# Kernel tuning notes

Measured on AMD Instinct MI355X. Metric: run time of the kernel, lower is better.

## Reference

```python
import jax, jax.numpy as jnp
import numpy as np

N_OP, N_TAB, N_COL, N_PRED = 131072, 32768, 131072, 65536
NCF = 32
H = 512
NUM_GRAPHS = 64
EPS = 1e-5  # torch LayerNorm default
# fixed relation order: (src_type, dst_type)
RELS = [('table', 'operator'), ('predicate', 'operator'), ('column', 'operator'),
        ('column', 'predicate'), ('operator', 'operator'), ('table', 'table'), ('column', 'column')]
NNODE = {'operator': N_OP, 'table': N_TAB, 'column': N_COL, 'predicate': N_PRED}
EDGES = [262144, 262144, 262144, 262144, 262144, 32768, 131072]


def setup_inputs() -> dict:
    key = jax.random.key(0)
    ks = iter(jax.random.split(key, 80))
    def nrm(shape, fan_in):
        return jax.random.normal(next(ks), shape, jnp.float32) / np.sqrt(fan_in).astype(np.float32)
    inp = {
        'x_operator': jax.random.normal(next(ks), (N_OP, 4), jnp.float32),
        'x_table': jax.random.normal(next(ks), (N_TAB, 2), jnp.float32),
        'x_column': jax.random.normal(next(ks), (N_COL, NCF), jnp.float32),
        'x_predicate': jax.random.normal(next(ks), (N_PRED, 4), jnp.float32),
        'W_op': nrm((4, H), 4), 'b_op': jnp.zeros((H,), jnp.float32),
        'W_tab': nrm((2, H), 2), 'b_tab': jnp.zeros((H,), jnp.float32),
        'W_col': nrm((NCF, H), NCF), 'b_col': jnp.zeros((H,), jnp.float32),
        'W_pred': nrm((4, H), 4), 'b_pred': jnp.zeros((H,), jnp.float32),
        'conv1_Wl': nrm((7, H, H), H), 'conv1_bl': jnp.zeros((7, H), jnp.float32),
        'conv1_Wr': nrm((7, H, H), H),
        'conv2_Wl': nrm((7, H, H), H), 'conv2_bl': jnp.zeros((7, H), jnp.float32),
        'conv2_Wr': nrm((7, H, H), H),
        'g1': jnp.ones((H,), jnp.float32), 'beta1': jnp.zeros((H,), jnp.float32),
        'g2': jnp.ones((H,), jnp.float32), 'beta2': jnp.zeros((H,), jnp.float32),
        'W_out': nrm((H, 1), H), 'b_out': jnp.zeros((1,), jnp.float32),
    }
    for i, (s, d) in enumerate(RELS):
        e = EDGES[i]
        inp[f'src{i}'] = jax.random.randint(next(ks), (e,), 0, NNODE[s], jnp.int32)
        inp[f'dst{i}'] = jax.random.randint(next(ks), (e,), 0, NNODE[d], jnp.int32)
    inp['batch_operator'] = jnp.sort(jax.random.randint(next(ks), (N_OP,), 0, NUM_GRAPHS, jnp.int32))
    return inp


def _layer_norm(x, g, b):
    m = jnp.mean(x, -1, keepdims=True)
    v = jnp.mean((x - m) ** 2, -1, keepdims=True)
    return (x - m) * jax.lax.rsqrt(v + EPS) * g + b


def _segment_mean(vals, idx, n):
    s = jax.ops.segment_sum(vals, idx, num_segments=n)
    c = jax.ops.segment_sum(jnp.ones(idx.shape, vals.dtype), idx, num_segments=n)
    return s / jnp.maximum(c, 1.0)[:, None]


def _sage(x_src, x_dst, src, dst, Wl, bl, Wr, n_dst):
    # PyG SAGEConv: lin_l(mean of neighbor msgs) + lin_r(root), lin_r has no bias
    agg = _segment_mean(x_src[src], dst, n_dst)
    return agg @ Wl + bl + x_dst @ Wr


def _forward(x_operator, x_table, x_column, x_predicate,
             W_op, b_op, W_tab, b_tab, W_col, b_col, W_pred, b_pred,
             conv1_Wl, conv1_bl, conv1_Wr, conv2_Wl, conv2_bl, conv2_Wr,
             g1, beta1, g2, beta2, W_out, b_out, edges, batch_operator):
    h = {'operator': x_operator @ W_op + b_op,
         'table': x_table @ W_tab + b_tab,
         'column': x_column @ W_col + b_col,
         'predicate': x_predicate @ W_pred + b_pred}

    def hetero(h, Wl, bl, Wr):
        outs = {}
        for i, (s, d) in enumerate(RELS):
            src, dst = edges[i]
            o = _sage(h[s], h[d], src, dst, Wl[i], bl[i], Wr[i], NNODE[d])
            outs.setdefault(d, []).append(o)
        # HeteroConv aggr='mean' across relations sharing a dst node type
        return {k: sum(v) / len(v) for k, v in outs.items()}

    h = hetero(h, conv1_Wl, conv1_bl, conv1_Wr)
    h = {k: _layer_norm(jax.nn.elu(v), g1, beta1) for k, v in h.items()}  # dropout = eval identity
    h = hetero(h, conv2_Wl, conv2_bl, conv2_Wr)
    h = {k: _layer_norm(jax.nn.elu(v), g2, beta2) for k, v in h.items()}
    pooled = _segment_mean(h['operator'], batch_operator, NUM_GRAPHS)  # global_mean_pool
    return (pooled @ W_out + b_out).squeeze()


def reference(x_operator, x_table, x_column, x_predicate,
              W_op, b_op, W_tab, b_tab, W_col, b_col, W_pred, b_pred,
              conv1_Wl, conv1_bl, conv1_Wr, conv2_Wl, conv2_bl, conv2_Wr,
              g1, beta1, g2, beta2, W_out, b_out,
              src0, dst0, src1, dst1, src2, dst2, src3, dst3,
              src4, dst4, src5, dst5, src6, dst6, batch_operator):
    edges = [(src0, dst0), (src1, dst1), (src2, dst2), (src3, dst3),
             (src4, dst4), (src5, dst5), (src6, dst6)]
    return _forward(x_operator, x_table, x_column, x_predicate,
                    W_op, b_op, W_tab, b_tab, W_col, b_col, W_pred, b_pred,
                    conv1_Wl, conv1_bl, conv1_Wr, conv2_Wl, conv2_bl, conv2_Wr,
                    g1, beta1, g2, beta2, W_out, b_out, edges, batch_operator)
```

## Files before the change

### kernel.cpp

```cpp
#include <hip/hip_runtime.h>
#include <hip/hip_bf16.h>

typedef unsigned short u16;
typedef __attribute__((ext_vector_type(8))) short bf16x8;
typedef __attribute__((ext_vector_type(4))) short bf16x4;
typedef __attribute__((ext_vector_type(4))) float f32x4;

typedef __attribute__((address_space(1))) const void gv_t;
typedef __attribute__((address_space(3))) void lv_t;

#define DEVINL __device__ __forceinline__

DEVINL float bf2f(u16 s) { union { unsigned u; float f; } v; v.u = ((unsigned)s) << 16; return v.f; }
DEVINL u16 f2bf(float f) {
  union { float f; unsigned u; } v; v.f = f;
  return (u16)((v.u + 0x7FFFu + ((v.u >> 16) & 1u)) >> 16);
}

__global__ void probe_k(float* __restrict__ out, float v) { out[threadIdx.x] = v; }

struct PackPtrs { const float* wl2; const float* wr2; const float* g1; u16* bt[5]; };
__global__ __launch_bounds__(256) void pack_multi(PackPtrs p) {
  int j = blockIdx.x >> 10;
  int idx = (blockIdx.x & 1023) * 256 + threadIdx.x;
  int k = idx >> 9, n = idx & 511;
  float v;
  if (j < 4) {
    int r = (j == 3) ? 4 : j;
    v = p.wl2[((size_t)r * 512 + k) * 512 + n];
  } else {
    size_t o = (size_t)k * 512 + n;
    v = p.wr2[o] + p.wr2[o + 262144] + p.wr2[o + 524288] + p.wr2[o + 1048576];
  }
  p.bt[j][(size_t)n * 512 + k] = f2bf(v * 0.25f * p.g1[k]);
}

__global__ __launch_bounds__(256) void csbb_k(const float* __restrict__ wl2,
                                              const float* __restrict__ wr2,
                                              const float* __restrict__ g1,
                                              const float* __restrict__ be1,
                                              float* __restrict__ cs, float* __restrict__ bb) {
  __shared__ float redA[256], redB[256];
  int j = blockIdx.x >> 4;
  int n = (blockIdx.x & 15) * 32 + (threadIdx.x & 31);
  int kg = threadIdx.x >> 5;
  float a = 0.f, b = 0.f;
  for (int k = kg * 64; k < kg * 64 + 64; ++k) {
    float w;
    if (j < 4) {
      int r = (j == 3) ? 4 : j;
      w = wl2[((size_t)r * 512 + k) * 512 + n];
    } else {
      size_t o = (size_t)k * 512 + n;
      w = wr2[o] + wr2[o + 262144] + wr2[o + 524288] + wr2[o + 1048576];
    }
    a += g1[k] * w;
    b += be1[k] * w;
  }
  redA[threadIdx.x] = a;
  redB[threadIdx.x] = b;
  __syncthreads();
  if (kg == 0) {
    float va = 0.f, vb = 0.f;
#pragma unroll
    for (int q = 0; q < 8; ++q) {
      va += redA[(threadIdx.x & 31) + q * 32];
      vb += redB[(threadIdx.x & 31) + q * 32];
    }
    cs[j * 512 + n] = va * 0.25f;
    bb[j * 512 + n] = vb * 0.25f;
  }
}

struct FoldPtrs { const float* a[8]; const float* w[2]; u16* bt[4]; };
__constant__ int   c_off[19] = {0,16,24,56,64,320,328,360,368,400,416,424,440,696,704,960,1216,1224,1256};
__constant__ int   c_ai[18]  = {0,1,2,3,4,5,6,7,6, 0,1,0, 4,5,4, 4,5,2};
__constant__ int   c_wi[18]  = {0,0,0,0,0,0,0,0,1, 0,0,1, 0,0,1, 0,0,1};
__constant__ int   c_r0[18]  = {0,0,1,1,2,2,4,4,0, 5,5,5, 6,6,6, 3,3,3};
__constant__ float c_sc[18]  = {0.25f,0.25f,0.25f,0.25f,0.25f,0.25f,0.25f,0.25f,0.25f,
                                1.f,1.f,1.f, 1.f,1.f,1.f, 1.f,1.f,1.f};
__constant__ int   c_bt[18]  = {0,0,0,0,0,0,0,0,0, 1,1,1, 2,2,2, 3,3,3};
__constant__ int   c_K[18]   = {64,64,64,64,64,64,64,64,64, 64,64,64, 128,128,128, 64,64,64};
__constant__ int   c_ko[18]  = {0,2,3,7,8,40,41,45,46, 0,2,3, 0,32,33, 0,32,33};

__global__ __launch_bounds__(256) void fold_multi(FoldPtrs p) {
  __shared__ float red[256];
  int b = blockIdx.x;
  int j = 0;
#pragma unroll
  for (int t = 1; t < 18; ++t) j += (b >= c_off[t]);
  int rel = b - c_off[j];
  int f = rel >> 3, nb = rel & 7;
  int tid = threadIdx.x;
  int n = nb * 64 + (tid & 63);
  int kg = tid >> 6;
  const float* A = p.a[c_ai[j]] + (size_t)f * 512;
  const float* W = p.w[c_wi[j]];
  int k0 = kg * 128;
  float acc = 0.f;
  if (j != 8) {
    const float* Wp = W + (size_t)c_r0[j] * 512 * 512 + n;
#pragma unroll 16
    for (int k = k0; k < k0 + 128; ++k) acc += A[k] * Wp[(size_t)k * 512];
  } else {
    const float* W0 = W + n;
    const float* W1 = W + (size_t)262144 + n;
    const float* W2 = W + (size_t)524288 + n;
    const float* W4 = W + (size_t)1048576 + n;
#pragma unroll 8
    for (int k = k0; k < k0 + 128; ++k) {
      size_t o = (size_t)k * 512;
      acc += A[k] * (W0[o] + W1[o] + W2[o] + W4[o]);
    }
  }
  red[tid] = acc;
  __syncthreads();
  if (kg == 0) {
    float v = red[tid] + red[tid + 64] + red[tid + 128] + red[tid + 192];
    p.bt[c_bt[j]][(size_t)n * c_K[j] + c_ko[j] + f] = f2bf(v * c_sc[j]);
  }
}

struct VFPtrs { const float* bl[5]; const float* bvec[5]; const float* w; float* out[5]; };
__constant__ int   c_vi[5][4] = {{0,1,2,4},{0,1,2,4},{5,-1,-1,-1},{6,-1,-1,-1},{3,-1,-1,-1}};
__constant__ float c_vs[5]    = {0.25f,0.25f,1.f,1.f,1.f};

__global__ __launch_bounds__(256) void vecfold_multi(VFPtrs p) {
  __shared__ float red[256];
  int j = blockIdx.x >> 4, blk = blockIdx.x & 15;
  int tid = threadIdx.x;
  int n = blk * 32 + (tid & 31);
  int kg = tid >> 5;
  const float* bv = p.bvec[j];
  float a = 0.f;
  if (bv) {
    int i1 = c_vi[j][1];
    const float* W0 = p.w + (size_t)c_vi[j][0] * 262144 + n;
    if (i1 < 0) {
#pragma unroll 16
      for (int k = kg * 64; k < kg * 64 + 64; ++k) a += bv[k] * W0[(size_t)k * 512];
    } else {
      const float* W1 = p.w + (size_t)c_vi[j][1] * 262144 + n;
      const float* W2 = p.w + (size_t)c_vi[j][2] * 262144 + n;
      const float* W3 = p.w + (size_t)c_vi[j][3] * 262144 + n;
#pragma unroll 8
      for (int k = kg * 64; k < kg * 64 + 64; ++k) {
        size_t o = (size_t)k * 512;
        a += bv[k] * (W0[o] + W1[o] + W2[o] + W3[o]);
      }
    }
  }
  red[tid] = a;
  __syncthreads();
  if (kg == 0) {
    float v = 0.f;
#pragma unroll
    for (int q = 0; q < 8; ++q) v += red[(tid & 31) + q * 32];
    float bsum = p.bl[j][c_vi[j][0] * 512 + n];
    if (c_vi[j][1] >= 0) {
      bsum += p.bl[j][c_vi[j][1] * 512 + n];
      bsum += p.bl[j][c_vi[j][2] * 512 + n];
      bsum += p.bl[j][c_vi[j][3] * 512 + n];
    }
    p.out[j][n] = (v + bsum) * c_vs[j];
  }
}

struct EdgePtrs { const int* dst[7]; const int* src[7]; };
__constant__ int c_hoff[8]  = {0,1024,2048,3072,4096,5120,5248,5760};
__constant__ int c_hbase[7] = {0,131072,262144,393216,458752,589824,622592};
__constant__ int c_hne[7]   = {262144,262144,262144,262144,262144,32768,131072};

__global__ __launch_bounds__(256) void hist_multi(EdgePtrs p, int* __restrict__ cnt) {
  int b = blockIdx.x;
  int j = 0;
#pragma unroll
  for (int t = 1; t < 7; ++t) j += (b >= c_hoff[t]);
  int i = (b - c_hoff[j]) * 256 + threadIdx.x;
  if (i < c_hne[j]) atomicAdd(&cnt[c_hbase[j] + p.dst[j][i]], 1);
}

__global__ __launch_bounds__(256) void fill_multi(EdgePtrs p, int* __restrict__ cursor,
                                                  int* __restrict__ esrc) {
  int b = blockIdx.x;
  int j = 0;
#pragma unroll
  for (int t = 1; t < 7; ++t) j += (b >= c_hoff[t]);
  int i = (b - c_hoff[j]) * 256 + threadIdx.x;
  if (i < c_hne[j]) {
    int pos = atomicAdd(&cursor[c_hbase[j] + p.dst[j][i]], 1);
    esrc[pos] = p.src[j][i];
  }
}

__global__ void scan1_k(const int* __restrict__ in, int* __restrict__ out,
                        int* __restrict__ part, int n) {
  __shared__ int s[256];
  int t = threadIdx.x;
  int base = blockIdx.x * 1024 + t * 4;
  int x0 = 0, x1 = 0, x2 = 0, x3 = 0;
  if (base < n) x0 = in[base];
  if (base + 1 < n) x1 = in[base + 1];
  if (base + 2 < n) x2 = in[base + 2];
  if (base + 3 < n) x3 = in[base + 3];
  int tsum = x0 + x1 + x2 + x3;
  s[t] = tsum;
  __syncthreads();
  for (int off = 1; off < 256; off <<= 1) {
    int v = (t >= off) ? s[t - off] : 0;
    __syncthreads();
    s[t] += v;
    __syncthreads();
  }
  int excl = s[t] - tsum;
  if (base < n) out[base] = excl;
  if (base + 1 < n) out[base + 1] = excl + x0;
  if (base + 2 < n) out[base + 2] = excl + x0 + x1;
  if (base + 3 < n) out[base + 3] = excl + x0 + x1 + x2;
  if (t == 255) part[blockIdx.x] = s[255];
}

__global__ void scan2_k(int* __restrict__ part, int nb) {
  __shared__ int s[1024];
  int t = threadIdx.x;
  int orig = (t < nb) ? part[t] : 0;
  s[t] = orig;
  __syncthreads();
  for (int off = 1; off < 1024; off <<= 1) {
    int v = (t >= off) ? s[t - off] : 0;
    __syncthreads();
    s[t] += v;
    __syncthreads();
  }
  if (t < nb) part[t] = s[t] - orig;
}

__global__ void scan3_k(int* __restrict__ out, int* __restrict__ cursor,
                        const int* __restrict__ part, int n) {
  int i = blockIdx.x * 256 + threadIdx.x;
  if (i < n) {
    int v = out[i] + part[i >> 10];
    out[i] = v;
    cursor[i] = v;
  }
}

__global__ void raw_agg(const int* __restrict__ offs, const int* __restrict__ esrc,
                        const float* __restrict__ x, int F, u16* __restrict__ A1,
                        int K, int colOff, int indCol, int nd) {
  int row = blockIdx.x * 32 + (threadIdx.x >> 3);
  if (row >= nd) return;
  int j = threadIdx.x & 7;
  int e0 = offs[row], e1 = offs[row + 1];
  float acc[4] = {0.f, 0.f, 0.f, 0.f};
  for (int e = e0; e < e1; ++e) {
    int s = esrc[e];
#pragma unroll
    for (int u = 0; u < 4; ++u) {
      int f = j + u * 8;
      if (f < F) acc[u] += x[(size_t)s * F + f];
    }
  }
  float inv = (e1 > e0) ? 1.f / (float)(e1 - e0) : 0.f;
#pragma unroll
  for (int u = 0; u < 4; ++u) {
    int f = j + u * 8;
    if (f < F) A1[(size_t)row * K + colOff + f] = f2bf(acc[u] * inv);
  }
  if (j == 0) A1[(size_t)row * K + indCol] = f2bf((e1 > e0) ? 1.f : 0.f);
}

struct RawPtrs { const int* offs; const int* esrc; const float* x[4]; u16* A1; };
__constant__ int c_gF[4]    = {2,4,32,4};
__constant__ int c_gco[4]   = {0,3,8,41};
__constant__ int c_gic[4]   = {2,7,40,45};
__constant__ int c_gcsrb[4] = {0,131072,262144,458752};

__global__ __launch_bounds__(256) void raw_multi(RawPtrs p, int s0) {
  int j = blockIdx.x >> 10;
  int row = (blockIdx.x & 1023) * 32 + (threadIdx.x >> 3);
  int jj = threadIdx.x & 7;
  const int* offs = p.offs + c_gcsrb[j] + s0;
  const float* x = p.x[j];
  int F = c_gF[j];
  int e0 = offs[row], e1 = offs[row + 1];
  float acc[4] = {0.f, 0.f, 0.f, 0.f};
  for (int e = e0; e < e1; ++e) {
    int s = p.esrc[e];
#pragma unroll
    for (int u = 0; u < 4; ++u) {
      int f = jj + u * 8;
      if (f < F) acc[u] += x[(size_t)s * F + f];
    }
  }
  float inv = (e1 > e0) ? 1.f / (float)(e1 - e0) : 0.f;
#pragma unroll
  for (int u = 0; u < 4; ++u) {
    int f = jj + u * 8;
    if (f < F) p.A1[(size_t)row * 64 + c_gco[j] + f] = f2bf(acc[u] * inv);
  }
  if (jj == 0) p.A1[(size_t)row * 64 + c_gic[j]] = f2bf((e1 > e0) ? 1.f : 0.f);
}

__global__ void a1_root(const float* __restrict__ x, int rowBase, u16* __restrict__ A1,
                        int K, int rootOff, int nd, int lf) {
  int idx = blockIdx.x * 256 + threadIdx.x;
  int i = idx >> lf, f = idx & ((1 << lf) - 1);
  if (i >= nd) return;
  A1[(size_t)i * K + rootOff + f] = f2bf(x[(((size_t)(rowBase + i)) << lf) + f]);
}

template <bool FIRST>
__global__ __launch_bounds__(256) void gather_acc(
    const int* __restrict__ offs, const int* __restrict__ esrc,
    const u16* __restrict__ hT, const float* __restrict__ bias,
    u16* __restrict__ acc, int s0, int s1) {
  int w = blockIdx.x * 4 + (threadIdx.x >> 6);
  int l = threadIdx.x & 63;
  int e0 = offs[w], e1 = offs[w + 1];
  float sum[8] = {0.f, 0.f, 0.f, 0.f, 0.f, 0.f, 0.f, 0.f};
  bool found = false;
  for (int e = e0; e < e1; ++e) {
    int s = esrc[e];
    if (s >= s0 && s < s1) {
      found = true;
      bf16x8 v = *(const bf16x8*)&hT[(size_t)(s - s0) * 512 + l * 8];
#pragma unroll
      for (int j = 0; j < 8; ++j) sum[j] += bf2f((u16)v[j]);
    }
  }
  float inv = (e1 > e0) ? 1.f / (float)(e1 - e0) : 0.f;
  u16* ap = acc + (size_t)w * 512 + l * 8;
  bf16x8 r;
  if (FIRST) {
#pragma unroll
    for (int j = 0; j < 8; ++j) r[j] = (short)f2bf(bias[l * 8 + j] + sum[j] * inv);
    *(bf16x8*)ap = r;
  } else {
    if (!found) return;
    bf16x8 old = *(const bf16x8*)ap;
#pragma unroll
    for (int j = 0; j < 8; ++j) r[j] = (short)f2bf(bf2f((u16)old[j]) + sum[j] * inv);
    *(bf16x8*)ap = r;
  }
}

template <bool ELU, int K>
__global__ __launch_bounds__(256) void gemm_k(
    const u16* __restrict__ A, const u16* __restrict__ BT,
    const float* __restrict__ bias, u16* __restrict__ C) {
  __shared__ u16 As[128 * 64];
  __shared__ u16 Bs[128 * 64];
  int b = blockIdx.x;
  int u = (b & 7) * 128 + (b >> 3);
  int bm = (u >> 2) * 128;
  int bn = (u & 3) * 128;
  int tid = threadIdx.x;
  int wid = tid >> 6, lane = tid & 63;
  int wm = wid >> 1, wn = wid & 1;
  int r16 = lane & 15, hi4 = lane >> 4;
  int srow = tid >> 3;
  int scol = ((tid & 7) ^ (srow & 7)) * 8;
  int sw = r16 & 7;
  f32x4 acc[4][4];
#pragma unroll
  for (int i = 0; i < 4; ++i)
#pragma unroll
    for (int j = 0; j < 4; ++j) acc[i][j] = (f32x4){0.f, 0.f, 0.f, 0.f};

#pragma unroll
  for (int k0 = 0; k0 < K; k0 += 64) {
    __syncthreads();
#pragma unroll
    for (int i = 0; i < 4; ++i) {
      const u16* ga = A + (size_t)(bm + i * 32 + srow) * K + k0 + scol;
      const u16* gb = BT + (size_t)(bn + i * 32 + srow) * K + k0 + scol;
      __builtin_amdgcn_global_load_lds((gv_t*)ga, (lv_t*)(As + i * 2048 + wid * 512), 16, 0, 0);
      __builtin_amdgcn_global_load_lds((gv_t*)gb, (lv_t*)(Bs + i * 2048 + wid * 512), 16, 0, 0);
    }
    __syncthreads();
#pragma unroll
    for (int kk = 0; kk < 64; kk += 32) {
      bf16x8 af[4], bfr[4];
#pragma unroll
      for (int f = 0; f < 4; ++f) {
        int grp = (kk >> 3) + hi4;
        af[f]  = *(const bf16x8*)&As[(wm * 64 + f * 16 + r16) * 64 + ((grp ^ sw) << 3)];
        bfr[f] = *(const bf16x8*)&Bs[(wn * 64 + f * 16 + r16) * 64 + ((grp ^ sw) << 3)];
      }
#pragma unroll
      for (int mf = 0; mf < 4; ++mf)
#pragma unroll
        for (int nf = 0; nf < 4; ++nf)
          acc[mf][nf] = __builtin_amdgcn_mfma_f32_16x16x32_bf16(bfr[nf], af[mf], acc[mf][nf], 0, 0, 0);
    }
  }
#pragma unroll
  for (int mf = 0; mf < 4; ++mf) {
    int r = bm + wm * 64 + mf * 16 + r16;
#pragma unroll
    for (int nf = 0; nf < 4; ++nf) {
      int c0 = bn + wn * 64 + nf * 16 + hi4 * 4;
      u16* cp = C + (size_t)r * 512 + c0;
      f32x4 bv = *(const f32x4*)&bias[c0];
      bf16x4 res;
#pragma unroll
      for (int j = 0; j < 4; ++j) {
        float v = acc[mf][nf][j] + bv[j];
        if (ELU) v = v > 0.f ? v : expm1f(v);
        res[j] = (short)f2bf(v);
      }
      *(bf16x4*)cp = res;
    }
  }
}

__global__ void ln_stats(const u16* __restrict__ H, float2* __restrict__ stats, int rows) {
  int w = blockIdx.x * 4 + (threadIdx.x >> 6);
  if (w >= rows) return;
  int l = threadIdx.x & 63;
  bf16x8 v = *(const bf16x8*)&H[(size_t)w * 512 + l * 8];
  float x[8];
  float s = 0.f;
#pragma unroll
  for (int j = 0; j < 8; ++j) { x[j] = bf2f((u16)v[j]); s += x[j]; }
#pragma unroll
  for (int m = 1; m < 64; m <<= 1) s += __shfl_xor(s, m, 64);
  float mean = s * (1.f / 512.f);
  float q = 0.f;
#pragma unroll
  for (int j = 0; j < 8; ++j) { float d = x[j] - mean; q += d * d; }
#pragma unroll
  for (int m = 1; m < 64; m <<= 1) q += __shfl_xor(q, m, 64);
  if (l == 0) stats[w] = make_float2(mean, rsqrtf(q * (1.f / 512.f) + 1e-5f));
}

template <bool ACC>
__global__ __launch_bounds__(256) void gemm_t(
    const u16* __restrict__ A, const u16* __restrict__ BT, u16* __restrict__ C,
    const float2* __restrict__ stats, const float* __restrict__ cs,
    const float* __restrict__ bb) {
  __shared__ u16 As[128 * 64];
  __shared__ u16 Bs[128 * 64];
  int b = blockIdx.x;
  int u = (b & 7) * 128 + (b >> 3);
  int bm = (u >> 2) * 128;
  int bn = (u & 3) * 128;
  int tid = threadIdx.x;
  int wid = tid >> 6, lane = tid & 63;
  int wm = wid >> 1, wn = wid & 1;
  int r16 = lane & 15, hi4 = lane >> 4;
  int srow = tid >> 3;
  int scol = ((tid & 7) ^ (srow & 7)) * 8;
  int sw = r16 & 7;
  f32x4 acc[4][4];
#pragma unroll
  for (int i = 0; i < 4; ++i)
#pragma unroll
    for (int j = 0; j < 4; ++j) acc[i][j] = (f32x4){0.f, 0.f, 0.f, 0.f};

#pragma unroll
  for (int k0 = 0; k0 < 512; k0 += 64) {
    __syncthreads();
#pragma unroll
    for (int i = 0; i < 4; ++i) {
      const u16* ga = A + (size_t)(bm + i * 32 + srow) * 512 + k0 + scol;
      const u16* gb = BT + (size_t)(bn + i * 32 + srow) * 512 + k0 + scol;
      __builtin_amdgcn_global_load_lds((gv_t*)ga, (lv_t*)(As + i * 2048 + wid * 512), 16, 0, 0);
      __builtin_amdgcn_global_load_lds((gv_t*)gb, (lv_t*)(Bs + i * 2048 + wid * 512), 16, 0, 0);
    }
    __syncthreads();
#pragma unroll
    for (int kk = 0; kk < 64; kk += 32) {
      bf16x8 af[4], bfr[4];
#pragma unroll
      for (int f = 0; f < 4; ++f) {
        int grp = (kk >> 3) + hi4;
        af[f]  = *(const bf16x8*)&As[(wm * 64 + f * 16 + r16) * 64 + ((grp ^ sw) << 3)];
        bfr[f] = *(const bf16x8*)&Bs[(wn * 64 + f * 16 + r16) * 64 + ((grp ^ sw) << 3)];
      }
#pragma unroll
      for (int mf = 0; mf < 4; ++mf)
#pragma unroll
        for (int nf = 0; nf < 4; ++nf)
          acc[mf][nf] = __builtin_amdgcn_mfma_f32_16x16x32_bf16(bfr[nf], af[mf], acc[mf][nf], 0, 0, 0);
    }
  }
#pragma unroll
  for (int mf = 0; mf < 4; ++mf) {
    int r = bm + wm * 64 + mf * 16 + r16;
    float2 st = stats[r];
    float mr = st.x * st.y;
#pragma unroll
    for (int nf = 0; nf < 4; ++nf) {
      int c0 = bn + wn * 64 + nf * 16 + hi4 * 4;
      u16* cp = C + (size_t)r * 512 + c0;
      f32x4 csv = *(const f32x4*)&cs[c0];
      f32x4 bbv = *(const f32x4*)&bb[c0];
      bf16x4 res;
      if (ACC) {
        bf16x4 oldv = *(const bf16x4*)cp;
#pragma unroll
        for (int j = 0; j < 4; ++j) {
          float v = st.y * acc[mf][nf][j] - mr * csv[j] + bbv[j] + bf2f((u16)oldv[j]);
          res[j] = (short)f2bf(v);
        }
      } else {
#pragma unroll
        for (int j = 0; j < 4; ++j) {
          float v = st.y * acc[mf][nf][j] - mr * csv[j] + bbv[j];
          res[j] = (short)f2bf(v);
        }
      }
      *(bf16x4*)cp = res;
    }
  }
}

DEVINL int lowb(const int* a, int n, int v) {
  int lo = 0, hi = n;
  while (lo < hi) { int m = (lo + hi) >> 1; if (a[m] < v) lo = m + 1; else hi = m; }
  return lo;
}

__global__ __launch_bounds__(256) void pool1v(const u16* __restrict__ H,
                                              const int* __restrict__ batch, int nOp,
                                              const float* __restrict__ g2,
                                              const float* __restrict__ be2,
                                              float* __restrict__ pooled,
                                              int* __restrict__ cnts) {
  __shared__ float red[4][512];
  int gr = blockIdx.x >> 4, part = blockIdx.x & 15;
  int lo = lowb(batch, nOp, gr), hi = lowb(batch, nOp, gr + 1);
  if (part == 0 && threadIdx.x == 0) cnts[gr] = hi - lo;
  int len = hi - lo;
  int chunk = (len + 15) >> 4;
  int r0 = lo + part * chunk;
  int r1 = r0 + chunk;
  if (r1 > hi) r1 = hi;
  int wv = threadIdx.x >> 6, l = threadIdx.x & 63;
  float a[8] = {0.f, 0.f, 0.f, 0.f, 0.f, 0.f, 0.f, 0.f};
  float gv[8], bv[8];
#pragma unroll
  for (int j = 0; j < 8; ++j) { gv[j] = g2[l * 8 + j]; bv[j] = be2[l * 8 + j]; }
  for (int r = r0 + wv; r < r1; r += 4) {
    bf16x8 v = *(const bf16x8*)&H[(size_t)r * 512 + l * 8];
    float x[8];
    float s = 0.f;
#pragma unroll
    for (int j = 0; j < 8; ++j) {
      x[j] = bf2f((u16)v[j]);
      x[j] = x[j] > 0.f ? x[j] : expm1f(x[j]);
      s += x[j];
    }
#pragma unroll
    for (int m = 1; m < 64; m <<= 1) s += __shfl_xor(s, m, 64);
    float mean = s * (1.f / 512.f);
    float q = 0.f;
#pragma unroll
    for (int j = 0; j < 8; ++j) { float d = x[j] - mean; q += d * d; }
#pragma unroll
    for (int m = 1; m < 64; m <<= 1) q += __shfl_xor(q, m, 64);
    float rsd = rsqrtf(q * (1.f / 512.f) + 1e-5f);
#pragma unroll
    for (int j = 0; j < 8; ++j) a[j] += (x[j] - mean) * rsd * gv[j] + bv[j];
  }
#pragma unroll
  for (int j = 0; j < 8; ++j) red[wv][l * 8 + j] = a[j];
  __syncthreads();
  if (wv == 0) {
#pragma unroll
    for (int j = 0; j < 8; ++j) {
      int c = l * 8 + j;
      float s = red[0][c] + red[1][c] + red[2][c] + red[3][c];
      atomicAdd(&pooled[gr * 512 + c], s);
    }
  }
}

__global__ void pool2(const float* __restrict__ pooled, const int* __restrict__ cnts,
                      const float* __restrict__ Wout, const float* __restrict__ bout,
                      float* __restrict__ out) {
  int gg = blockIdx.x;
  int l = threadIdx.x;
  float s = 0.f;
#pragma unroll
  for (int j = 0; j < 8; ++j) {
    int c = l * 8 + j;
    s += pooled[gg * 512 + c] * Wout[c];
  }
#pragma unroll
  for (int m = 1; m < 64; m <<= 1) s += __shfl_xor(s, m, 64);
  if (l == 0) {
    int c = cnts[gg];
    if (c < 1) c = 1;
    out[gg] = s / (float)c + bout[0];
  }
}

extern "C" void kernel_launch(void* const* d_in, const int* in_sizes, int n_in,
                              void* d_out, int out_size, void* d_ws, size_t ws_size,
                              hipStream_t stream) {
  (void)in_sizes; (void)n_in; (void)out_size;
  const float* x_op   = (const float*)d_in[0];
  const float* x_tab  = (const float*)d_in[1];
  const float* x_col  = (const float*)d_in[2];
  const float* x_pred = (const float*)d_in[3];
  const float* W_op = (const float*)d_in[4],  *b_op = (const float*)d_in[5];
  const float* W_tab = (const float*)d_in[6], *b_tab = (const float*)d_in[7];
  const float* W_col = (const float*)d_in[8], *b_col = (const float*)d_in[9];
  const float* W_pred = (const float*)d_in[10], *b_pred = (const float*)d_in[11];
  const float* Wl1 = (const float*)d_in[12];
  const float* bl1 = (const float*)d_in[13];
  const float* Wr1 = (const float*)d_in[14];
  const float* Wl2 = (const float*)d_in[15];
  const float* bl2 = (const float*)d_in[16];
  const float* Wr2 = (const float*)d_in[17];
  const float* g1  = (const float*)d_in[18];
  const float* be1 = (const float*)d_in[19];
  const float* g2  = (const float*)d_in[20];
  const float* be2 = (const float*)d_in[21];
  const float* Wout = (const float*)d_in[22];
  const float* bout = (const float*)d_in[23];
  const int* SRC[7], *DST[7];
  for (int r = 0; r < 7; ++r) { SRC[r] = (const int*)d_in[24 + 2 * r]; DST[r] = (const int*)d_in[25 + 2 * r]; }
  const int* batch = (const int*)d_in[38];
  float* out = (float*)d_out;

  const int CSRB[7] = {0, 131072, 262144, 393216, 458752, 589824, 622592};
  const int TOT = 753664;
  const int NOP = 131072;

  char* ws = (char*)d_ws;
  u16* acc     = (u16*)ws;
  u16* h1      = (u16*)(ws + 134217728ull);
  int* curFul  = (int*)(ws + 134217728ull);
  u16* hT      = (u16*)(ws + 167772160ull);
  u16* A1      = (u16*)(ws + 234881024ull);
  int* offsFul = (int*)(ws + 243269632ull);
  int* esrcFul = (int*)(ws + 246284544ull);
  u16* BT2_0   = (u16*)(ws + 252182784ull);
  u16* BT2_1   = BT2_0 + 262144;
  u16* BT2_2   = BT2_1 + 262144;
  u16* BT2_4   = BT2_2 + 262144;
  u16* BT2rt   = BT2_4 + 262144;
  u16* BT1op   = (u16*)(ws + 254804224ull);
  u16* BT1tab  = (u16*)(ws + 254869760ull);
  u16* BT1col  = (u16*)(ws + 254935296ull);
  u16* BT1pr   = (u16*)(ws + 255066368ull);
  float* b1op  = (float*)(ws + 255131904ull);
  float* b1tab = b1op + 512, *b1col = b1op + 1024, *b1pr = b1op + 1536, *b2vec = b1op + 2048;
  float* pooled = (float*)(ws + 255142144ull);
  int* cnts     = (int*)(ws + 255273216ull);
  int* part     = (int*)(ws + 255273472ull);
  float2* stats = (float2*)(ws + 255277568ull);
  float* cs     = (float*)(ws + 255539712ull);
  float* bb     = (float*)(ws + 255549952ull);
  const size_t WS_NEED = 255560192ull;
  if (ws_size < WS_NEED) { probe_k<<<1, 64, 0, stream>>>(out, (float)ws_size); return; }

  (void)hipMemsetAsync(curFul, 0, 3014912ull, stream);
  EdgePtrs ep;
  for (int r = 0; r < 7; ++r) { ep.dst[r] = DST[r]; ep.src[r] = SRC[r]; }
  hist_multi<<<5760, 256, 0, stream>>>(ep, curFul);
  scan1_k<<<737, 256, 0, stream>>>(curFul, offsFul, part, TOT + 1);
  scan2_k<<<1, 1024, 0, stream>>>(part, 737);
  scan3_k<<<2945, 256, 0, stream>>>(offsFul, curFul, part, TOT + 1);
  fill_multi<<<5760, 256, 0, stream>>>(ep, curFul, esrcFul);

  PackPtrs pp;
  pp.wl2 = Wl2; pp.wr2 = Wr2; pp.g1 = g1;
  pp.bt[0] = BT2_0; pp.bt[1] = BT2_1; pp.bt[2] = BT2_2; pp.bt[3] = BT2_4; pp.bt[4] = BT2rt;
  pack_multi<<<5120, 256, 0, stream>>>(pp);
  csbb_k<<<80, 256, 0, stream>>>(Wl2, Wr2, g1, be1, cs, bb);
  (void)hipMemsetAsync(BT1op, 0, 65536 + 65536 + 131072 + 65536, stream);
  FoldPtrs fp;
  fp.a[0] = W_tab; fp.a[1] = b_tab; fp.a[2] = W_pred; fp.a[3] = b_pred;
  fp.a[4] = W_col; fp.a[5] = b_col; fp.a[6] = W_op;   fp.a[7] = b_op;
  fp.w[0] = Wl1;   fp.w[1] = Wr1;
  fp.bt[0] = BT1op; fp.bt[1] = BT1tab; fp.bt[2] = BT1col; fp.bt[3] = BT1pr;
  fold_multi<<<1256, 256, 0, stream>>>(fp);
  VFPtrs vp;
  vp.bl[0] = bl2; vp.bl[1] = bl1; vp.bl[2] = bl1; vp.bl[3] = bl1; vp.bl[4] = bl1;
  vp.bvec[0] = nullptr; vp.bvec[1] = b_op; vp.bvec[2] = b_tab; vp.bvec[3] = b_col; vp.bvec[4] = b_pred;
  vp.w = Wr1;
  vp.out[0] = b2vec; vp.out[1] = b1op; vp.out[2] = b1tab; vp.out[3] = b1col; vp.out[4] = b1pr;
  vecfold_multi<<<80, 256, 0, stream>>>(vp);

  float* cs0 = cs, *cs1 = cs + 512, *cs2 = cs + 1024, *cs4 = cs + 1536, *csrt = cs + 2048;
  float* bb0 = bb, *bb1 = bb + 512, *bb2 = bb + 1024, *bb4 = bb + 1536, *bbrt = bb + 2048;

  (void)hipMemsetAsync(A1, 0, 32768ull * 64 * 2, stream);
  raw_agg<<<1024, 256, 0, stream>>>(offsFul + CSRB[5], esrcFul, x_tab, 2, A1, 64, 0, 2, 32768);
  a1_root<<<256, 256, 0, stream>>>(x_tab, 0, A1, 64, 3, 32768, 1);
  gemm_k<true, 64><<<1024, 256, 0, stream>>>(A1, BT1tab, b1tab, h1);
  ln_stats<<<8192, 256, 0, stream>>>(h1, stats, 32768);
  gemm_t<false><<<1024, 256, 0, stream>>>(h1, BT2_0, hT, stats, cs0, bb0);
  gather_acc<true><<<32768, 256, 0, stream>>>(offsFul + CSRB[0], esrcFul, hT, b2vec, acc, 0, 32768);

  (void)hipMemsetAsync(A1, 0, 32768ull * 64 * 2, stream);
  for (int q = 0; q < 2; ++q) {
    int qs = q * 32768;
    raw_agg<<<1024, 256, 0, stream>>>(offsFul + CSRB[3] + qs, esrcFul, x_col, 32, A1, 64, 0, 32, 32768);
    a1_root<<<512, 256, 0, stream>>>(x_pred, qs, A1, 64, 33, 32768, 2);
    gemm_k<true, 64><<<1024, 256, 0, stream>>>(A1, BT1pr, b1pr, h1);
    ln_stats<<<8192, 256, 0, stream>>>(h1, stats, 32768);
    gemm_t<false><<<1024, 256, 0, stream>>>(h1, BT2_1, hT + (size_t)qs * 512, stats, cs1, bb1);
  }
  gather_acc<false><<<32768, 256, 0, stream>>>(offsFul + CSRB[1], esrcFul, hT, nullptr, acc, 0, 65536);

  (void)hipMemsetAsync(A1, 0, 32768ull * 128 * 2, stream);
  for (int hs = 0; hs < 2; ++hs) {
    int S0 = hs * 65536;
    for (int q = 0; q < 2; ++q) {
      int qs = S0 + q * 32768;
      raw_agg<<<1024, 256, 0, stream>>>(offsFul + CSRB[6] + qs, esrcFul, x_col, 32, A1, 128, 0, 32, 32768);
      a1_root<<<4096, 256, 0, stream>>>(x_col, qs, A1, 128, 33, 32768, 5);
      gemm_k<true, 128><<<1024, 256, 0, stream>>>(A1, BT1col, b1col, h1);
      ln_stats<<<8192, 256, 0, stream>>>(h1, stats, 32768);
      gemm_t<false><<<1024, 256, 0, stream>>>(h1, BT2_2, hT + (size_t)q * 32768 * 512, stats, cs2, bb2);
    }
    gather_acc<false><<<32768, 256, 0, stream>>>(offsFul + CSRB[2], esrcFul, hT, nullptr,
                                                 acc, S0, S0 + 65536);
  }

  (void)hipMemsetAsync(A1, 0, 32768ull * 64 * 2, stream);
  for (int hs = 0; hs < 2; ++hs) {
    int S0 = hs * 65536;
    for (int q = 0; q < 2; ++q) {
      int qs = S0 + q * 32768;
      RawPtrs rp;
      rp.offs = offsFul; rp.esrc = esrcFul; rp.A1 = A1;
      rp.x[0] = x_tab; rp.x[1] = x_pred; rp.x[2] = x_col; rp.x[3] = x_op;
      raw_multi<<<4096, 256, 0, stream>>>(rp, qs);
      a1_root<<<512, 256, 0, stream>>>(x_op, qs, A1, 64, 46, 32768, 2);
      gemm_k<true, 64><<<1024, 256, 0, stream>>>(A1, BT1op, b1op, h1);
      ln_stats<<<8192, 256, 0, stream>>>(h1, stats, 32768);
      gemm_t<true><<<1024, 256, 0, stream>>>(h1, BT2rt, acc + (size_t)qs * 512, stats, csrt, bbrt);
      gemm_t<false><<<1024, 256, 0, stream>>>(h1, BT2_4, hT + (size_t)q * 32768 * 512, stats, cs4, bb4);
    }
    gather_acc<false><<<32768, 256, 0, stream>>>(offsFul + CSRB[4], esrcFul, hT, nullptr,
                                                 acc, S0, S0 + 65536);
  }

  (void)hipMemsetAsync(pooled, 0, 64 * 512 * 4, stream);
  pool1v<<<1024, 256, 0, stream>>>(acc, batch, NOP, g2, be2, pooled, cnts);
  pool2<<<64, 64, 0, stream>>>(pooled, cnts, Wout, bout, out);
}
```

Baseline: 1.614 ms.

## Partition CSR build atomics by destination range and merge operator gemm_t launches

The histogram and fill kernels now launch eight times as many blocks, and each block handles only edges whose destination index falls in one of eight ranges. The aim is to keep each block's atomics on a narrower, more cache-local region of the counter array, at the cost of every edge index being read eight times. Separately, the two gemm_t launches for the operator root and operator-operator relation are fused into one 2048-block kernel, which removes a launch and lets both GEMMs run concurrently on the same h1 input.

Result: faster. 1.561 ms (-3.3%).

```diff
diff --git a/kernel.cpp b/kernel.cpp
--- a/kernel.cpp
+++ b/kernel.cpp
@@ -171,25 +171,37 @@
 __constant__ int c_hbase[7] = {0,131072,262144,393216,458752,589824,622592};
 __constant__ int c_hne[7]   = {262144,262144,262144,262144,262144,32768,131072};
 
-__global__ __launch_bounds__(256) void hist_multi(EdgePtrs p, int* __restrict__ cnt) {
-  int b = blockIdx.x;
-  int j = 0;
-#pragma unroll
-  for (int t = 1; t < 7; ++t) j += (b >= c_hoff[t]);
-  int i = (b - c_hoff[j]) * 256 + threadIdx.x;
-  if (i < c_hne[j]) atomicAdd(&cnt[c_hbase[j] + p.dst[j][i]], 1);
-}
-
-__global__ __launch_bounds__(256) void fill_multi(EdgePtrs p, int* __restrict__ cursor,
-                                                  int* __restrict__ esrc) {
-  int b = blockIdx.x;
-  int j = 0;
-#pragma unroll
-  for (int t = 1; t < 7; ++t) j += (b >= c_hoff[t]);
-  int i = (b - c_hoff[j]) * 256 + threadIdx.x;
-  if (i < c_hne[j]) {
-    int pos = atomicAdd(&cursor[c_hbase[j] + p.dst[j][i]], 1);
-    esrc[pos] = p.src[j][i];
+__global__ __launch_bounds__(256) void hist8(EdgePtrs p, int* __restrict__ cnt) {
+  int range = blockIdx.x & 7;
+  int lo = range * 94208, hi = lo + 94208;
+  for (int chunk = blockIdx.x >> 3; chunk < 5760; chunk += 4096) {
+    int j = 0;
+#pragma unroll
+    for (int t = 1; t < 7; ++t) j += (chunk >= c_hoff[t]);
+    int i = (chunk - c_hoff[j]) * 256 + threadIdx.x;
+    if (i < c_hne[j]) {
+      int idx = c_hbase[j] + p.dst[j][i];
+      if (idx >= lo && idx < hi) atomicAdd(&cnt[idx], 1);
+    }
+  }
+}
+
+__global__ __launch_bounds__(256) void fill8(EdgePtrs p, int* __restrict__ cursor,
+                                             int* __restrict__ esrc) {
+  int range = blockIdx.x & 7;
+  int lo = range * 94208, hi = lo + 94208;
+  for (int chunk = blockIdx.x >> 3; chunk < 5760; chunk += 4096) {
+    int j = 0;
+#pragma unroll
+    for (int t = 1; t < 7; ++t) j += (chunk >= c_hoff[t]);
+    int i = (chunk - c_hoff[j]) * 256 + threadIdx.x;
+    if (i < c_hne[j]) {
+      int idx = c_hbase[j] + p.dst[j][i];
+      if (idx >= lo && idx < hi) {
+        int pos = atomicAdd(&cursor[idx], 1);
+        esrc[pos] = p.src[j][i];
+      }
+    }
   }
 }
 
@@ -499,6 +511,93 @@
       f32x4 bbv = *(const f32x4*)&bb[c0];
       bf16x4 res;
       if (ACC) {
+        bf16x4 oldv = *(const bf16x4*)cp;
+#pragma unroll
+        for (int j = 0; j < 4; ++j) {
+          float v = st.y * acc[mf][nf][j] - mr * csv[j] + bbv[j] + bf2f((u16)oldv[j]);
+          res[j] = (short)f2bf(v);
+        }
+      } else {
+#pragma unroll
+        for (int j = 0; j < 4; ++j) {
+          float v = st.y * acc[mf][nf][j] - mr * csv[j] + bbv[j];
+          res[j] = (short)f2bf(v);
+        }
+      }
+      *(bf16x4*)cp = res;
+    }
+  }
+}
+
+__global__ __launch_bounds__(256) void gemm_t2(
+    const u16* __restrict__ A, const u16* __restrict__ BTrt, const u16* __restrict__ BT4,
+    u16* __restrict__ Cacc, u16* __restrict__ ChT, const float2* __restrict__ stats,
+    const float* __restrict__ csrt, const float* __restrict__ bbrt,
+    const float* __restrict__ cs4, const float* __restrict__ bb4) {
+  __shared__ u16 As[128 * 64];
+  __shared__ u16 Bs[128 * 64];
+  bool second = blockIdx.x >= 1024;
+  const u16* BT = second ? BT4 : BTrt;
+  u16* C = second ? ChT : Cacc;
+  const float* cs = second ? cs4 : csrt;
+  const float* bb = second ? bb4 : bbrt;
+  int b = blockIdx.x & 1023;
+  int u = (b & 7) * 128 + (b >> 3);
+  int bm = (u >> 2) * 128;
+  int bn = (u & 3) * 128;
+  int tid = threadIdx.x;
+  int wid = tid >> 6, lane = tid & 63;
+  int wm = wid >> 1, wn = wid & 1;
+  int r16 = lane & 15, hi4 = lane >> 4;
+  int srow = tid >> 3;
+  int scol = ((tid & 7) ^ (srow & 7)) * 8;
+  int sw = r16 & 7;
+  f32x4 acc[4][4];
+#pragma unroll
+  for (int i = 0; i < 4; ++i)
+#pragma unroll
+    for (int j = 0; j < 4; ++j) acc[i][j] = (f32x4){0.f, 0.f, 0.f, 0.f};
+
+#pragma unroll
+  for (int k0 = 0; k0 < 512; k0 += 64) {
+    __syncthreads();
+#pragma unroll
+    for (int i = 0; i < 4; ++i) {
+      const u16* ga = A + (size_t)(bm + i * 32 + srow) * 512 + k0 + scol;
+      const u16* gb = BT + (size_t)(bn + i * 32 + srow) * 512 + k0 + scol;
+      __builtin_amdgcn_global_load_lds((gv_t*)ga, (lv_t*)(As + i * 2048 + wid * 512), 16, 0, 0);
+      __builtin_amdgcn_global_load_lds((gv_t*)gb, (lv_t*)(Bs + i * 2048 + wid * 512), 16, 0, 0);
+    }
+    __syncthreads();
+#pragma unroll
+    for (int kk = 0; kk < 64; kk += 32) {
+      bf16x8 af[4], bfr[4];
+#pragma unroll
+      for (int f = 0; f < 4; ++f) {
+        int grp = (kk >> 3) + hi4;
+        af[f]  = *(const bf16x8*)&As[(wm * 64 + f * 16 + r16) * 64 + ((grp ^ sw) << 3)];
+        bfr[f] = *(const bf16x8*)&Bs[(wn * 64 + f * 16 + r16) * 64 + ((grp ^ sw) << 3)];
+      }
+#pragma unroll
+      for (int mf = 0; mf < 4; ++mf)
+#pragma unroll
+        for (int nf = 0; nf < 4; ++nf)
+          acc[mf][nf] = __builtin_amdgcn_mfma_f32_16x16x32_bf16(bfr[nf], af[mf], acc[mf][nf], 0, 0, 0);
+    }
+  }
+#pragma unroll
+  for (int mf = 0; mf < 4; ++mf) {
+    int r = bm + wm * 64 + mf * 16 + r16;
+    float2 st = stats[r];
+    float mr = st.x * st.y;
+#pragma unroll
+    for (int nf = 0; nf < 4; ++nf) {
+      int c0 = bn + wn * 64 + nf * 16 + hi4 * 4;
+      u16* cp = C + (size_t)r * 512 + c0;
+      f32x4 csv = *(const f32x4*)&cs[c0];
+      f32x4 bbv = *(const f32x4*)&bb[c0];
+      bf16x4 res;
+      if (!second) {
         bf16x4 oldv = *(const bf16x4*)cp;
 #pragma unroll
         for (int j = 0; j < 4; ++j) {
@@ -662,11 +761,11 @@
   (void)hipMemsetAsync(curFul, 0, 3014912ull, stream);
   EdgePtrs ep;
   for (int r = 0; r < 7; ++r) { ep.dst[r] = DST[r]; ep.src[r] = SRC[r]; }
-  hist_multi<<<5760, 256, 0, stream>>>(ep, curFul);
+  hist8<<<32768, 256, 0, stream>>>(ep, curFul);
   scan1_k<<<737, 256, 0, stream>>>(curFul, offsFul, part, TOT + 1);
   scan2_k<<<1, 1024, 0, stream>>>(part, 737);
   scan3_k<<<2945, 256, 0, stream>>>(offsFul, curFul, part, TOT + 1);
-  fill_multi<<<5760, 256, 0, stream>>>(ep, curFul, esrcFul);
+  fill8<<<32768, 256, 0, stream>>>(ep, curFul, esrcFul);
 
   PackPtrs pp;
   pp.wl2 = Wl2; pp.wr2 = Wr2; pp.g1 = g1;
@@ -736,8 +835,9 @@
       a1_root<<<512, 256, 0, stream>>>(x_op, qs, A1, 64, 46, 32768, 2);
       gemm_k<true, 64><<<1024, 256, 0, stream>>>(A1, BT1op, b1op, h1);
       ln_stats<<<8192, 256, 0, stream>>>(h1, stats, 32768);
-      gemm_t<true><<<1024, 256, 0, stream>>>(h1, BT2rt, acc + (size_t)qs * 512, stats, csrt, bbrt);
-      gemm_t<false><<<1024, 256, 0, stream>>>(h1, BT2_4, hT + (size_t)q * 32768 * 512, stats, cs4, bb4);
+      gemm_t2<<<2048, 256, 0, stream>>>(h1, BT2rt, BT2_4, acc + (size_t)qs * 512,
+                                        hT + (size_t)q * 32768 * 512, stats,
+                                        csrt, bbrt, cs4, bb4);
     }
     gather_acc<false><<<32768, 256, 0, stream>>>(offsFul + CSRB[4], esrcFul, hT, nullptr,
                                                  acc, S0, S0 + 65536);
```
